# Optimization experiments

Hardware: AMD Instinct MI355X
Metric: run time of the kernel (lower is better)

Reference implementation:

```python
import jax, jax.numpy as jnp
import numpy as np

QBITS = 8  # all quant points configured to 8-bit symmetric by default


def fake_quant(v, bits=QBITS):
    """Symmetric per-tensor fake quantize/dequantize with STE-compatible form."""
    qmax = float(2 ** (bits - 1) - 1)
    scale = jnp.maximum(jnp.max(jnp.abs(v)) / qmax, 1e-8)
    q = jnp.clip(jnp.round(v / scale), -qmax - 1.0, qmax) * scale
    # straight-through estimator (identity gradient)
    return v + jax.lax.stop_gradient(q - v)


def reorder_pt_to_haste(w):
    # PyTorch gate order (r,z,n) -> Haste order (z,r,n) along leading 3H axis
    h3 = w.shape[0] // 3
    return jnp.concatenate([w[h3:2 * h3], w[:h3], w[2 * h3:]], axis=0)


def setup_inputs() -> dict:
    key = jax.random.key(0)
    ks = jax.random.split(key, 6)
    T, B, I, H = 1024, 64, 256, 256
    s = 1.0 / np.sqrt(H)
    return {
        "x": jax.random.normal(ks[0], (T, B, I), dtype=jnp.float32),
        "weight_ih": jax.random.normal(ks[1], (3 * H, I), dtype=jnp.float32) * s,
        "weight_hh": jax.random.normal(ks[2], (3 * H, H), dtype=jnp.float32) * s,
        "bias_ih": jax.random.normal(ks[3], (3 * H,), dtype=jnp.float32) * s,
        "bias_hh": jax.random.normal(ks[4], (3 * H,), dtype=jnp.float32) * s,
        "h0": jax.random.normal(ks[5], (B, H), dtype=jnp.float32),
    }


def _quant_gru(x, weight_ih, weight_hh, bias_ih, bias_hh, h0):
    T, B, I = x.shape
    H = weight_hh.shape[1]
    # Haste layout: W [I,3H], R [H,3H], gate order (z,r,n)
    W = reorder_pt_to_haste(weight_ih).T   # [I, 3H]
    R = reorder_pt_to_haste(weight_hh).T   # [H, 3H]
    bx = reorder_pt_to_haste(bias_ih)      # [3H]
    br = reorder_pt_to_haste(bias_hh)      # [3H]

    # per-tensor fake quant of inputs / weights / biases
    xq = fake_quant(x)
    Wq = fake_quant(W)
    Rq = fake_quant(R)
    bxq = fake_quant(bx)
    brq = fake_quant(br)

    # precompute Wx for all timesteps: [T,B,3H], quantized matmul output
    Wx = fake_quant(jnp.einsum('tbi,ih->tbh', xq, Wq))

    bx_z, bx_r, bx_n = bxq[:H], bxq[H:2 * H], bxq[2 * H:]
    br_z, br_r, br_n = brq[:H], brq[H:2 * H], brq[2 * H:]

    def step(h, wx_t):
        hq = fake_quant(h)
        Rh = fake_quant(hq @ Rq)           # [B, 3H]
        Rh_z, Rh_r, Rh_n = Rh[:, :H], Rh[:, H:2 * H], Rh[:, 2 * H:]
        wx_z, wx_r, wx_n = wx_t[:, :H], wx_t[:, H:2 * H], wx_t[:, 2 * H:]

        z_pre = fake_quant(wx_z + bx_z + Rh_z + br_z)
        z = fake_quant(jax.nn.sigmoid(z_pre))
        r_pre = fake_quant(wx_r + bx_r + Rh_r + br_r)
        r = fake_quant(jax.nn.sigmoid(r_pre))

        Rh_add_br = fake_quant(Rh_n + br_n)
        rRh = fake_quant(r * Rh_add_br)
        g_pre = fake_quant(wx_n + bx_n + rRh)
        g = fake_quant(jnp.tanh(g_pre))

        old_contrib = fake_quant(z * h)
        new_contrib = fake_quant((1.0 - z) * g)
        h_new = old_contrib + new_contrib
        return h_new, h_new

    h_last, output = jax.lax.scan(step, h0, Wx)  # output: [T, B, H]
    return output, h_last[None]  # h_n: [1, B, H]


def reference(x, weight_ih, weight_hh, bias_ih, bias_hh, h0):
    return _quant_gru(x, weight_ih, weight_hh, bias_ih, bias_hh, h0)
```

## Files before the change

kernel.cpp:

```cpp
#include <hip/hip_runtime.h>
#include <cstdint>
#include <cstddef>


typedef int   v4i __attribute__((ext_vector_type(4)));
typedef float v4f __attribute__((ext_vector_type(4)));

#define T_STEPS 1024
#define OUT_MAIN_FLOATS (1024*64*256)
#define WXQ_DOUT_OFF 16842752

__device__ __forceinline__ float clamp128(float x) {
  return fminf(fmaxf(x, -128.0f), 127.0f);
}
__device__ __forceinline__ int permj(int j) {
  return j < 256 ? j + 256 : (j < 512 ? j - 256 : j);
}
__device__ __forceinline__ float sigmoidf_(float x) {
  return __fdividef(1.0f, 1.0f + __expf(-x));
}
__device__ __forceinline__ float tanhf_(float x) {
  float e = __expf(-2.0f * fabsf(x));
  float t = __fdividef(1.0f - e, 1.0f + e);
  return copysignf(t, x);
}
__device__ __forceinline__ unsigned skey(float x) {
  unsigned u = __float_as_uint(x);
  return (u & 0x80000000u) ? ~u : (u | 0x80000000u);
}
__device__ __forceinline__ float sdec(unsigned k) {
  unsigned u = (k & 0x80000000u) ? (k ^ 0x80000000u) : ~k;
  return __uint_as_float(u);
}
__device__ __forceinline__ float wave_amax(float v) {
  #pragma unroll
  for (int m = 1; m <= 32; m <<= 1) v = fmaxf(v, __shfl_xor(v, m, 64));
  return v;
}

#define MFMA_I8(a, b, c) __builtin_amdgcn_mfma_i32_16x16x64_i8(a, b, c, 0, 0, 0)

__global__ void k_absmax(const float* __restrict__ p, int n4, unsigned* slot) {
  int i = blockIdx.x * blockDim.x + threadIdx.x;
  int stride = gridDim.x * blockDim.x;
  const v4f* p4 = (const v4f*)p;
  float m = 0.0f;
  for (; i < n4; i += stride) {
    v4f v = p4[i];
    m = fmaxf(m, fmaxf(fmaxf(fabsf(v[0]), fabsf(v[1])),
                       fmaxf(fabsf(v[2]), fabsf(v[3]))));
  }
  m = wave_amax(m);
  if ((threadIdx.x & 63) == 0) atomicMax(slot, __float_as_uint(m));
}

__global__ void k_frag(const float* __restrict__ src,
                       const unsigned* __restrict__ slots, int slot_idx,
                       signed char* __restrict__ dst) {
  int id = blockIdx.x * 256 + threadIdx.x;
  float s = fmaxf(__uint_as_float(slots[slot_idx]) / 127.0f, 1e-8f);
  int bq   = id & 3;
  int lane = (id >> 2) & 63;
  int kc   = (id >> 8) & 3;
  int ct   = id >> 10;
  int n = ct * 16 + (lane & 15);
  int k = kc * 64 + (lane >> 4) * 16 + bq * 4;
  const float* p = src + permj(n) * 256 + k;
  int b0 = ((int)clamp128(rintf(p[0] / s))) & 255;
  int b1 = ((int)clamp128(rintf(p[1] / s))) & 255;
  int b2 = ((int)clamp128(rintf(p[2] / s))) & 255;
  int b3 = ((int)clamp128(rintf(p[3] / s))) & 255;
  ((int*)dst)[id] = b0 | (b1 << 8) | (b2 << 16) | (b3 << 24);
}

__global__ void k_bias(const float* __restrict__ bih, const float* __restrict__ bhh,
                       const unsigned* __restrict__ slots, float* __restrict__ bqo) {
  int j = threadIdx.x;
  float s_bx = fmaxf(__uint_as_float(slots[3]) / 127.0f, 1e-8f);
  float s_br = fmaxf(__uint_as_float(slots[4]) / 127.0f, 1e-8f);
  int pr = permj(j);
  bqo[j]       = s_bx * clamp128(rintf(bih[pr] / s_bx));
  bqo[768 + j] = s_br * clamp128(rintf(bhh[pr] / s_br));
}

__global__ void k_xq(const float* __restrict__ x, const unsigned* __restrict__ slots,
                     signed char* __restrict__ xq8, int n4) {
  int i = blockIdx.x * blockDim.x + threadIdx.x;
  if (i >= n4) return;
  float s_x = fmaxf(__uint_as_float(slots[0]) / 127.0f, 1e-8f);
  v4f v = ((const v4f*)x)[i];
  int b0 = ((int)clamp128(rintf(v[0] / s_x))) & 255;
  int b1 = ((int)clamp128(rintf(v[1] / s_x))) & 255;
  int b2 = ((int)clamp128(rintf(v[2] / s_x))) & 255;
  int b3 = ((int)clamp128(rintf(v[3] / s_x))) & 255;
  ((int*)xq8)[i] = b0 | (b1 << 8) | (b2 << 16) | (b3 << 24);
}

__global__ __launch_bounds__(1024) void k_wx_i8(
    const signed char* __restrict__ xq8, const signed char* __restrict__ wf,
    unsigned* __restrict__ slots, signed char* __restrict__ wxq, int mode) {
  const int t = blockIdx.x;
  const int tid = threadIdx.x, lane = tid & 63, w = tid >> 6;
  const int cl = lane & 15, lh = lane >> 4;

  v4i Bz[4], Br[4], Bn[4];
  #pragma unroll
  for (int kc = 0; kc < 4; ++kc) {
    Bz[kc] = *(const v4i*)(wf + (((w)*4      + kc) * 64 + lane) * 16);
    Br[kc] = *(const v4i*)(wf + (((w + 16)*4 + kc) * 64 + lane) * 16);
    Bn[kc] = *(const v4i*)(wf + (((w + 32)*4 + kc) * 64 + lane) * 16);
  }
  v4i acc[3][4];
  #pragma unroll
  for (int p = 0; p < 3; ++p)
    #pragma unroll
    for (int rt = 0; rt < 4; ++rt) acc[p][rt] = (v4i){0, 0, 0, 0};

  const signed char* xr = xq8 + t * 16384;
  #pragma unroll
  for (int kc = 0; kc < 4; ++kc)
    #pragma unroll
    for (int rt = 0; rt < 4; ++rt) {
      v4i A = *(const v4i*)(xr + (rt * 16 + cl) * 256 + kc * 64 + lh * 16);
      acc[0][rt] = MFMA_I8(A, Bz[kc], acc[0][rt]);
      acc[1][rt] = MFMA_I8(A, Br[kc], acc[1][rt]);
      acc[2][rt] = MFMA_I8(A, Bn[kc], acc[2][rt]);
    }

  if (mode == 0) {
    int mm = 0;
    #pragma unroll
    for (int p = 0; p < 3; ++p)
      #pragma unroll
      for (int rt = 0; rt < 4; ++rt)
        #pragma unroll
        for (int rg = 0; rg < 4; ++rg) mm = max(mm, abs(acc[p][rt][rg]));
    #pragma unroll
    for (int m = 1; m <= 32; m <<= 1) mm = max(mm, __shfl_xor(mm, m, 64));
    if (lane == 0) atomicMax((int*)(slots + 5), mm);
  } else {
    int islot = *(const int*)(slots + 5);
    float maxMf = (float)islot;
    float s_x = fmaxf(__uint_as_float(slots[0]) / 127.0f, 1e-8f);
    float s_W = fmaxf(__uint_as_float(slots[1]) / 127.0f, 1e-8f);
    float s_xW = s_x * s_W;
    float s_wx = fmaxf(s_xW * maxMf / 127.0f, 1e-8f);
    #pragma unroll
    for (int p = 0; p < 3; ++p)
      #pragma unroll
      for (int rt = 0; rt < 4; ++rt) {
        int dw = 0;
        #pragma unroll
        for (int rg = 0; rg < 4; ++rg) {
          float qf = clamp128(rintf((s_xW * (float)acc[p][rt][rg]) / s_wx));
          dw |= (((int)qf) & 255) << (rg * 8);
        }
        ((int*)wxq)[t * 12288 + p * 4096 + rt * 1024 + w * 64 + lh * 16 + cl] = dw;
      }
  }
}

template <int NCH>
__device__ __forceinline__ void xchg(unsigned* keys, unsigned tag,
    unsigned (*lred)[8], unsigned long long* gslot, int wg, int tid, int lane) {
  const int rset = tag % 3;
  #pragma unroll
  for (int c = 0; c < NCH; ++c) {
    unsigned v = keys[c];
    #pragma unroll
    for (int m = 1; m <= 32; m <<= 1)
      v = max(v, (unsigned)__shfl_xor((int)v, m, 64));
    keys[c] = v;
  }
  if (lane == 0) {
    #pragma unroll
    for (int c = 0; c < NCH; ++c) atomicMax(&lred[rset][c], keys[c]);
  }
  __syncthreads();
  const int par = tag & 1;
  if (tid < NCH) {
    unsigned long long v =
        ((unsigned long long)tag << 32) | (unsigned long long)lred[rset][tid];
    __hip_atomic_store(&gslot[(par * 4 + wg) * 8 + tid], v,
                       __ATOMIC_RELAXED, __HIP_MEMORY_SCOPE_AGENT);
  } else if (tid == 32) {
    int ns = rset + 1; if (ns == 3) ns = 0;
    #pragma unroll
    for (int c = 0; c < 8; ++c) lred[ns][c] = 0u;
  } else if (tid >= 64 && tid < 64 + 3 * NCH) {
    int idx = tid - 64;
    int owi = idx / NCH;
    int c = idx - owi * NCH;
    int ow = owi + (owi >= wg ? 1 : 0);
    unsigned long long* p = &gslot[(par * 4 + ow) * 8 + c];
    unsigned long long v;
    do {
      v = __hip_atomic_load(p, __ATOMIC_RELAXED, __HIP_MEMORY_SCOPE_AGENT);
    } while ((unsigned)(v >> 32) != tag);
    atomicMax(&lred[rset][c], (unsigned)v);
  }
  __syncthreads();
  #pragma unroll
  for (int c = 0; c < NCH; ++c) keys[c] = lred[rset][c];
}

__global__ __launch_bounds__(1024) void k_recur4b(
    const signed char* __restrict__ wxq, const signed char* __restrict__ brf,
    const float* __restrict__ bq, const unsigned* __restrict__ slots,
    const float* __restrict__ h0p, float* __restrict__ out,
    unsigned long long* __restrict__ gslot) {
  __shared__ signed char ah[16 * 272];
  __shared__ unsigned lred[3][8];

  const int tid = threadIdx.x;
  const int lane = tid & 63;
  const int w = tid >> 6;
  const int cl = lane & 15;
  const int lh = lane >> 4;
  const int wg = blockIdx.x;
  const int j = w * 16 + cl;
  const int brow = wg * 16 + lh * 4;

  if (tid < 24) ((unsigned*)lred)[tid] = 0u;

  float s_x = fmaxf(__uint_as_float(slots[0]) / 127.0f, 1e-8f);
  float s_W = fmaxf(__uint_as_float(slots[1]) / 127.0f, 1e-8f);
  float s_R = fmaxf(__uint_as_float(slots[2]) / 127.0f, 1e-8f);
  float maxM0 = (float)(*(const int*)(slots + 5));
  float s_wx = fmaxf(s_x * s_W * maxM0 / 127.0f, 1e-8f);

  float bxz = bq[j], bxr = bq[j + 256], bxn = bq[j + 512];
  float brz = bq[768 + j], brr = bq[1024 + j], brn = bq[1280 + j];

  v4i Bz[4], Br[4], Bn[4];
  #pragma unroll
  for (int kc = 0; kc < 4; ++kc) {
    Bz[kc] = *(const v4i*)(brf + (((w)*4      + kc) * 64 + lane) * 16);
    Br[kc] = *(const v4i*)(brf + (((w + 16)*4 + kc) * 64 + lane) * 16);
    Bn[kc] = *(const v4i*)(brf + (((w + 32)*4 + kc) * 64 + lane) * 16);
  }

  float h[4];
  #pragma unroll
  for (int rg = 0; rg < 4; ++rg) h[rg] = h0p[(brow + rg) * 256 + j];

  __syncthreads();

  unsigned tag = 1;
  float sh;
  {
    float m = fmaxf(fmaxf(fabsf(h[0]), fabsf(h[1])),
                    fmaxf(fabsf(h[2]), fabsf(h[3])));
    unsigned kk[1] = {__float_as_uint(m)};
    xchg<1>(kk, tag++, lred, gslot, wg, tid, lane);
    sh = fmaxf(__uint_as_float(kk[0]) / 127.0f, 1e-8f);
    float ish = 1.0f / sh;
    #pragma unroll
    for (int rg = 0; rg < 4; ++rg)
      ah[(lh * 4 + rg) * 272 + j] = (signed char)(int)rintf(h[rg] * ish);
    __syncthreads();
  }

  for (int t = 0; t < T_STEPS; ++t) {
    const signed char* wb = wxq + (size_t)t * 49152 + (wg << 12) + (tid << 2);
    int wvz = *(const int*)(wb);
    int wvr = *(const int*)(wb + 16384);
    int wvn = *(const int*)(wb + 32768);

    v4i az4 = {0,0,0,0}, ar4 = {0,0,0,0}, an4 = {0,0,0,0};
    #pragma unroll
    for (int kc = 0; kc < 4; ++kc) {
      v4i A = *(const v4i*)(ah + cl * 272 + kc * 64 + lh * 16);
      az4 = MFMA_I8(A, Bz[kc], az4);
      ar4 = MFMA_I8(A, Br[kc], ar4);
      an4 = MFMA_I8(A, Bn[kc], an4);
    }

    int mm = 0;
    #pragma unroll
    for (int rg = 0; rg < 4; ++rg)
      mm = max(mm, max(abs(az4[rg]), max(abs(ar4[rg]), abs(an4[rg]))));
    unsigned kk[5];
    kk[0] = (unsigned)mm;
    xchg<1>(kk, tag++, lred, gslot, wg, tid, lane);
    float maxMf = (float)(int)kk[0];
    float s_Rh = fmaxf(sh * s_R * maxMf / 127.0f, 1e-8f);
    float fRh = (sh * s_R) / s_Rh;

    float zp[4], rp[4], nb[4];
    float az = 0.0f, ar = 0.0f, an = 0.0f;
    float mzs = -3.402823466e38f, mrs = -3.402823466e38f;
    #pragma unroll
    for (int rg = 0; rg < 4; ++rg) {
      float Rz = s_Rh * rintf((float)az4[rg] * fRh);
      float Rr = s_Rh * rintf((float)ar4[rg] * fRh);
      float Rn = s_Rh * rintf((float)an4[rg] * fRh);
      float wz = s_wx * (float)((signed char)(wvz >> (rg * 8)));
      float wr = s_wx * (float)((signed char)(wvr >> (rg * 8)));
      float a1 = ((wz + bxz) + Rz) + brz;
      float a2 = ((wr + bxr) + Rr) + brr;
      float a3 = Rn + brn;
      zp[rg] = a1; rp[rg] = a2; nb[rg] = a3;
      az = fmaxf(az, fabsf(a1)); ar = fmaxf(ar, fabsf(a2));
      an = fmaxf(an, fabsf(a3));
      mzs = fmaxf(mzs, a1); mrs = fmaxf(mrs, a2);
    }
    kk[0] = __float_as_uint(az); kk[1] = __float_as_uint(ar);
    kk[2] = __float_as_uint(an); kk[3] = skey(mzs); kk[4] = skey(mrs);
    xchg<5>(kk, tag++, lred, gslot, wg, tid, lane);
    float s1 = fmaxf(__uint_as_float(kk[0]) / 127.0f, 1e-8f), i1 = 1.0f / s1;
    float s2 = fmaxf(__uint_as_float(kk[1]) / 127.0f, 1e-8f), i2 = 1.0f / s2;
    float s3 = fmaxf(__uint_as_float(kk[2]) / 127.0f, 1e-8f), i3 = 1.0f / s3;
    float zq_max = s1 * rintf(sdec(kk[3]) * i1);
    float rq_max = s2 * rintf(sdec(kk[4]) * i2);
    float s4 = fmaxf(sigmoidf_(zq_max) / 127.0f, 1e-8f), i4 = 1.0f / s4;
    float s5 = fmaxf(sigmoidf_(rq_max) / 127.0f, 1e-8f), i5 = 1.0f / s5;

    float zf[4], rr_[4];
    float m6 = 0.0f;
    #pragma unroll
    for (int rg = 0; rg < 4; ++rg) {
      float zq = s1 * rintf(zp[rg] * i1);
      float rq = s2 * rintf(rp[rg] * i2);
      float zv = sigmoidf_(zq);
      float rv = sigmoidf_(rq);
      zf[rg] = s4 * rintf(zv * i4);
      float rq2 = s5 * rintf(rv * i5);
      float nbq = s3 * rintf(nb[rg] * i3);
      float rr = rq2 * nbq;
      rr_[rg] = rr;
      m6 = fmaxf(m6, fabsf(rr));
    }
    kk[0] = __float_as_uint(m6);
    xchg<1>(kk, tag++, lred, gslot, wg, tid, lane);
    float s6 = fmaxf(__uint_as_float(kk[0]) / 127.0f, 1e-8f), i6 = 1.0f / s6;

    float gp[4];
    float m7 = 0.0f;
    #pragma unroll
    for (int rg = 0; rg < 4; ++rg) {
      float rrq = s6 * rintf(rr_[rg] * i6);
      float wn = s_wx * (float)((signed char)(wvn >> (rg * 8)));
      float g = (wn + bxn) + rrq;
      gp[rg] = g;
      m7 = fmaxf(m7, fabsf(g));
    }
    kk[0] = __float_as_uint(m7);
    xchg<1>(kk, tag++, lred, gslot, wg, tid, lane);
    float m7g = __uint_as_float(kk[0]);
    float s7 = fmaxf(m7g / 127.0f, 1e-8f), i7 = 1.0f / s7;
    float gq_max = s7 * rintf(m7g * i7);
    float s8 = fmaxf(tanhf_(gq_max) / 127.0f, 1e-8f), i8v = 1.0f / s8;

    float ov[4], nv[4];
    float mo = 0.0f, mn = 0.0f;
    #pragma unroll
    for (int rg = 0; rg < 4; ++rg) {
      float gpq = s7 * rintf(gp[rg] * i7);
      float gv = tanhf_(gpq);
      float gq = s8 * rintf(gv * i8v);
      float o = zf[rg] * h[rg];
      float n = (1.0f - zf[rg]) * gq;
      ov[rg] = o; nv[rg] = n;
      mo = fmaxf(mo, fabsf(o)); mn = fmaxf(mn, fabsf(n));
    }
    kk[0] = __float_as_uint(mo); kk[1] = __float_as_uint(mn);
    xchg<2>(kk, tag++, lred, gslot, wg, tid, lane);
    float s9  = fmaxf(__uint_as_float(kk[0]) / 127.0f, 1e-8f), i9  = 1.0f / s9;
    float s10 = fmaxf(__uint_as_float(kk[1]) / 127.0f, 1e-8f), i10 = 1.0f / s10;

    float mh = 0.0f;
    #pragma unroll
    for (int rg = 0; rg < 4; ++rg) {
      float oq = s9  * rintf(ov[rg] * i9);
      float nq = s10 * rintf(nv[rg] * i10);
      float hn = oq + nq;
      h[rg] = hn;
      mh = fmaxf(mh, fabsf(hn));
      out[t * 16384 + (brow + rg) * 256 + j] = hn;
    }
    kk[0] = __float_as_uint(mh);
    xchg<1>(kk, tag++, lred, gslot, wg, tid, lane);
    sh = fmaxf(__uint_as_float(kk[0]) / 127.0f, 1e-8f);
    float ish = 1.0f / sh;
    #pragma unroll
    for (int rg = 0; rg < 4; ++rg)
      ah[(lh * 4 + rg) * 272 + j] = (signed char)(int)rintf(h[rg] * ish);
    __syncthreads();
  }

  #pragma unroll
  for (int rg = 0; rg < 4; ++rg)
    out[OUT_MAIN_FLOATS + (brow + rg) * 256 + j] = h[rg];
}

extern "C" void kernel_launch(void* const* d_in, const int* in_sizes, int n_in,
                              void* d_out, int out_size, void* d_ws, size_t ws_size,
                              hipStream_t stream) {
  const float* x   = (const float*)d_in[0];
  const float* wih = (const float*)d_in[1];
  const float* whh = (const float*)d_in[2];
  const float* bih = (const float*)d_in[3];
  const float* bhh = (const float*)d_in[4];
  const float* h0  = (const float*)d_in[5];
  float* out = (float*)d_out;

  unsigned* slots = (unsigned*)d_ws;
  unsigned long long* gslot = (unsigned long long*)((char*)d_ws + 512);
  float* bq       = (float*)((char*)d_ws + 4096);
  signed char* F  = (signed char*)d_ws + 10240;

  signed char* wxq = (signed char*)d_out + WXQ_DOUT_OFF;
  signed char* xq8 = (signed char*)d_out;

  hipMemsetAsync(d_ws, 0, 4096, stream);

  k_absmax<<<dim3(1024), dim3(256), 0, stream>>>(x,   16777216 / 4, slots + 0);
  k_absmax<<<dim3(96),   dim3(256), 0, stream>>>(wih, 196608 / 4,   slots + 1);
  k_absmax<<<dim3(96),   dim3(256), 0, stream>>>(whh, 196608 / 4,   slots + 2);
  k_absmax<<<dim3(1),    dim3(256), 0, stream>>>(bih, 768 / 4,      slots + 3);
  k_absmax<<<dim3(1),    dim3(256), 0, stream>>>(bhh, 768 / 4,      slots + 4);

  k_frag<<<dim3(192), dim3(256), 0, stream>>>(wih, slots, 1, F);
  k_bias<<<dim3(1), dim3(768), 0, stream>>>(bih, bhh, slots, bq);
  k_xq<<<dim3(16384), dim3(256), 0, stream>>>(x, slots, xq8, 4194304);

  k_wx_i8<<<dim3(1024), dim3(1024), 0, stream>>>(xq8, F, slots, wxq, 0);
  k_wx_i8<<<dim3(1024), dim3(1024), 0, stream>>>(xq8, F, slots, wxq, 1);

  k_frag<<<dim3(192), dim3(256), 0, stream>>>(whh, slots, 2, F);

  k_recur4b<<<dim3(4), dim3(1024), 0, stream>>>(wxq, F, bq, slots, h0, out,
                                                gslot);
}
```

Before: 14.14 ms.

## Split recurrent GRU kernel across 16 workgroups of 4 batch rows each

Re-partitions the sequential recurrence from 4 workgroups of 1024 threads (16 batch rows each) to 16 workgroups of 512 threads (4 batch rows each, padded to a 16-row MFMA tile with zeros). Each wave now computes two column tiles and stages MFMA results in shared memory so threads can handle 2 rows each. The grid-wide absmax exchange now waits on 15 peers instead of 3 per reduction. This spreads the per-step work over more compute units but wastes MFMA work on padding rows and raises cross-workgroup synchronization cost at each of the seven exchanges per step.

```diff
diff --git a/kernel.cpp b/kernel.cpp
--- a/kernel.cpp
+++ b/kernel.cpp
@@ -9,6 +9,7 @@
 #define T_STEPS 1024
 #define OUT_MAIN_FLOATS (1024*64*256)
 #define WXQ_DOUT_OFF 16842752
+#define NWG 16
 
 __device__ __forceinline__ float clamp128(float x) {
   return fminf(fmaxf(x, -128.0f), 127.0f);
@@ -181,18 +182,18 @@
   if (tid < NCH) {
     unsigned long long v =
         ((unsigned long long)tag << 32) | (unsigned long long)lred[rset][tid];
-    __hip_atomic_store(&gslot[(par * 4 + wg) * 8 + tid], v,
+    __hip_atomic_store(&gslot[(par * NWG + wg) * 8 + tid], v,
                        __ATOMIC_RELAXED, __HIP_MEMORY_SCOPE_AGENT);
   } else if (tid == 32) {
     int ns = rset + 1; if (ns == 3) ns = 0;
     #pragma unroll
     for (int c = 0; c < 8; ++c) lred[ns][c] = 0u;
-  } else if (tid >= 64 && tid < 64 + 3 * NCH) {
+  } else if (tid >= 64 && tid < 64 + (NWG - 1) * NCH) {
     int idx = tid - 64;
     int owi = idx / NCH;
     int c = idx - owi * NCH;
     int ow = owi + (owi >= wg ? 1 : 0);
-    unsigned long long* p = &gslot[(par * 4 + ow) * 8 + c];
+    unsigned long long* p = &gslot[(par * NWG + ow) * 8 + c];
     unsigned long long v;
     do {
       v = __hip_atomic_load(p, __ATOMIC_RELAXED, __HIP_MEMORY_SCOPE_AGENT);
@@ -204,12 +205,15 @@
   for (int c = 0; c < NCH; ++c) keys[c] = lred[rset][c];
 }
 
-__global__ __launch_bounds__(1024) void k_recur4b(
+__global__ __launch_bounds__(512, 1) void k_recur16(
     const signed char* __restrict__ wxq, const signed char* __restrict__ brf,
     const float* __restrict__ bq, const unsigned* __restrict__ slots,
     const float* __restrict__ h0p, float* __restrict__ out,
     unsigned long long* __restrict__ gslot) {
   __shared__ signed char ah[16 * 272];
+  __shared__ int zs[4 * 256];
+  __shared__ int rs_[4 * 256];
+  __shared__ int ns_[4 * 256];
   __shared__ unsigned lred[3][8];
 
   const int tid = threadIdx.x;
@@ -218,10 +222,11 @@
   const int cl = lane & 15;
   const int lh = lane >> 4;
   const int wg = blockIdx.x;
-  const int j = w * 16 + cl;
-  const int brow = wg * 16 + lh * 4;
+  const int j = tid & 255;
+  const int rp = (tid >> 8) * 2;
 
   if (tid < 24) ((unsigned*)lred)[tid] = 0u;
+  for (int i = tid; i < 1088; i += 512) ((int*)ah)[i] = 0;
 
   float s_x = fmaxf(__uint_as_float(slots[0]) / 127.0f, 1e-8f);
   float s_W = fmaxf(__uint_as_float(slots[1]) / 127.0f, 1e-8f);
@@ -232,54 +237,81 @@
   float bxz = bq[j], bxr = bq[j + 256], bxn = bq[j + 512];
   float brz = bq[768 + j], brr = bq[1024 + j], brn = bq[1280 + j];
 
-  v4i Bz[4], Br[4], Bn[4];
-  #pragma unroll
-  for (int kc = 0; kc < 4; ++kc) {
-    Bz[kc] = *(const v4i*)(brf + (((w)*4      + kc) * 64 + lane) * 16);
-    Br[kc] = *(const v4i*)(brf + (((w + 16)*4 + kc) * 64 + lane) * 16);
-    Bn[kc] = *(const v4i*)(brf + (((w + 32)*4 + kc) * 64 + lane) * 16);
-  }
-
-  float h[4];
-  #pragma unroll
-  for (int rg = 0; rg < 4; ++rg) h[rg] = h0p[(brow + rg) * 256 + j];
+  v4i Bz[2][4], Br[2][4], Bn[2][4];
+  #pragma unroll
+  for (int cg = 0; cg < 2; ++cg) {
+    int ct = w * 2 + cg;
+    #pragma unroll
+    for (int kc = 0; kc < 4; ++kc) {
+      Bz[cg][kc] = *(const v4i*)(brf + ((ct * 4        + kc) * 64 + lane) * 16);
+      Br[cg][kc] = *(const v4i*)(brf + (((ct + 16) * 4 + kc) * 64 + lane) * 16);
+      Bn[cg][kc] = *(const v4i*)(brf + (((ct + 32) * 4 + kc) * 64 + lane) * 16);
+    }
+  }
+
+  float h[2];
+  #pragma unroll
+  for (int s = 0; s < 2; ++s)
+    h[s] = h0p[(wg * 4 + rp + s) * 256 + j];
 
   __syncthreads();
 
   unsigned tag = 1;
   float sh;
   {
-    float m = fmaxf(fmaxf(fabsf(h[0]), fabsf(h[1])),
-                    fmaxf(fabsf(h[2]), fabsf(h[3])));
+    float m = fmaxf(fabsf(h[0]), fabsf(h[1]));
     unsigned kk[1] = {__float_as_uint(m)};
     xchg<1>(kk, tag++, lred, gslot, wg, tid, lane);
     sh = fmaxf(__uint_as_float(kk[0]) / 127.0f, 1e-8f);
     float ish = 1.0f / sh;
     #pragma unroll
-    for (int rg = 0; rg < 4; ++rg)
-      ah[(lh * 4 + rg) * 272 + j] = (signed char)(int)rintf(h[rg] * ish);
+    for (int s = 0; s < 2; ++s)
+      ah[(rp + s) * 272 + j] = (signed char)(int)rintf(h[s] * ish);
     __syncthreads();
   }
 
+  const int widx0 = (wg >> 2) * 1024 + (j >> 4) * 64 + (wg & 3) * 16 + (j & 15);
+
   for (int t = 0; t < T_STEPS; ++t) {
-    const signed char* wb = wxq + (size_t)t * 49152 + (wg << 12) + (tid << 2);
-    int wvz = *(const int*)(wb);
-    int wvr = *(const int*)(wb + 16384);
-    int wvn = *(const int*)(wb + 32768);
-
-    v4i az4 = {0,0,0,0}, ar4 = {0,0,0,0}, an4 = {0,0,0,0};
+    const int* wxi = (const int*)wxq + (size_t)t * 12288 + widx0;
+    int wvz = wxi[0];
+    int wvr = wxi[4096];
+    int wvn = wxi[8192];
+
+    v4i aZ[2] = {(v4i){0,0,0,0}, (v4i){0,0,0,0}};
+    v4i aR[2] = {(v4i){0,0,0,0}, (v4i){0,0,0,0}};
+    v4i aN[2] = {(v4i){0,0,0,0}, (v4i){0,0,0,0}};
     #pragma unroll
     for (int kc = 0; kc < 4; ++kc) {
       v4i A = *(const v4i*)(ah + cl * 272 + kc * 64 + lh * 16);
-      az4 = MFMA_I8(A, Bz[kc], az4);
-      ar4 = MFMA_I8(A, Br[kc], ar4);
-      an4 = MFMA_I8(A, Bn[kc], an4);
+      #pragma unroll
+      for (int cg = 0; cg < 2; ++cg) {
+        aZ[cg] = MFMA_I8(A, Bz[cg][kc], aZ[cg]);
+        aR[cg] = MFMA_I8(A, Br[cg][kc], aR[cg]);
+        aN[cg] = MFMA_I8(A, Bn[cg][kc], aN[cg]);
+      }
+    }
+
+    if (lane < 16) {
+      #pragma unroll
+      for (int cg = 0; cg < 2; ++cg) {
+        int jj = (w * 2 + cg) * 16 + lane;
+        #pragma unroll
+        for (int rg = 0; rg < 4; ++rg) {
+          zs[rg * 256 + jj] = aZ[cg][rg];
+          rs_[rg * 256 + jj] = aR[cg][rg];
+          ns_[rg * 256 + jj] = aN[cg][rg];
+        }
+      }
     }
 
     int mm = 0;
     #pragma unroll
-    for (int rg = 0; rg < 4; ++rg)
-      mm = max(mm, max(abs(az4[rg]), max(abs(ar4[rg]), abs(an4[rg]))));
+    for (int cg = 0; cg < 2; ++cg)
+      #pragma unroll
+      for (int rg = 0; rg < 4; ++rg)
+        mm = max(mm, max(abs(aZ[cg][rg]),
+                         max(abs(aR[cg][rg]), abs(aN[cg][rg]))));
     unsigned kk[5];
     kk[0] = (unsigned)mm;
     xchg<1>(kk, tag++, lred, gslot, wg, tid, lane);
@@ -287,20 +319,21 @@
     float s_Rh = fmaxf(sh * s_R * maxMf / 127.0f, 1e-8f);
     float fRh = (sh * s_R) / s_Rh;
 
-    float zp[4], rp[4], nb[4];
+    float zp[2], rpre[2], nb[2];
     float az = 0.0f, ar = 0.0f, an = 0.0f;
     float mzs = -3.402823466e38f, mrs = -3.402823466e38f;
     #pragma unroll
-    for (int rg = 0; rg < 4; ++rg) {
-      float Rz = s_Rh * rintf((float)az4[rg] * fRh);
-      float Rr = s_Rh * rintf((float)ar4[rg] * fRh);
-      float Rn = s_Rh * rintf((float)an4[rg] * fRh);
-      float wz = s_wx * (float)((signed char)(wvz >> (rg * 8)));
-      float wr = s_wx * (float)((signed char)(wvr >> (rg * 8)));
+    for (int s = 0; s < 2; ++s) {
+      int r = rp + s;
+      float Rz = s_Rh * rintf((float)zs[r * 256 + j] * fRh);
+      float Rr = s_Rh * rintf((float)rs_[r * 256 + j] * fRh);
+      float Rn = s_Rh * rintf((float)ns_[r * 256 + j] * fRh);
+      float wz = s_wx * (float)((signed char)(wvz >> (r * 8)));
+      float wr = s_wx * (float)((signed char)(wvr >> (r * 8)));
       float a1 = ((wz + bxz) + Rz) + brz;
       float a2 = ((wr + bxr) + Rr) + brr;
       float a3 = Rn + brn;
-      zp[rg] = a1; rp[rg] = a2; nb[rg] = a3;
+      zp[s] = a1; rpre[s] = a2; nb[s] = a3;
       az = fmaxf(az, fabsf(a1)); ar = fmaxf(ar, fabsf(a2));
       an = fmaxf(an, fabsf(a3));
       mzs = fmaxf(mzs, a1); mrs = fmaxf(mrs, a2);
@@ -316,33 +349,33 @@
     float s4 = fmaxf(sigmoidf_(zq_max) / 127.0f, 1e-8f), i4 = 1.0f / s4;
     float s5 = fmaxf(sigmoidf_(rq_max) / 127.0f, 1e-8f), i5 = 1.0f / s5;
 
-    float zf[4], rr_[4];
+    float zf[2], rr_[2];
     float m6 = 0.0f;
     #pragma unroll
-    for (int rg = 0; rg < 4; ++rg) {
-      float zq = s1 * rintf(zp[rg] * i1);
-      float rq = s2 * rintf(rp[rg] * i2);
+    for (int s = 0; s < 2; ++s) {
+      float zq = s1 * rintf(zp[s] * i1);
+      float rq = s2 * rintf(rpre[s] * i2);
       float zv = sigmoidf_(zq);
       float rv = sigmoidf_(rq);
-      zf[rg] = s4 * rintf(zv * i4);
+      zf[s] = s4 * rintf(zv * i4);
       float rq2 = s5 * rintf(rv * i5);
-      float nbq = s3 * rintf(nb[rg] * i3);
+      float nbq = s3 * rintf(nb[s] * i3);
       float rr = rq2 * nbq;
-      rr_[rg] = rr;
+      rr_[s] = rr;
       m6 = fmaxf(m6, fabsf(rr));
     }
     kk[0] = __float_as_uint(m6);
     xchg<1>(kk, tag++, lred, gslot, wg, tid, lane);
     float s6 = fmaxf(__uint_as_float(kk[0]) / 127.0f, 1e-8f), i6 = 1.0f / s6;
 
-    float gp[4];
+    float gp[2];
     float m7 = 0.0f;
     #pragma unroll
-    for (int rg = 0; rg < 4; ++rg) {
-      float rrq = s6 * rintf(rr_[rg] * i6);
-      float wn = s_wx * (float)((signed char)(wvn >> (rg * 8)));
+    for (int s = 0; s < 2; ++s) {
+      float rrq = s6 * rintf(rr_[s] * i6);
+      float wn = s_wx * (float)((signed char)(wvn >> ((rp + s) * 8)));
       float g = (wn + bxn) + rrq;
-      gp[rg] = g;
+      gp[s] = g;
       m7 = fmaxf(m7, fabsf(g));
     }
     kk[0] = __float_as_uint(m7);
@@ -352,16 +385,16 @@
     float gq_max = s7 * rintf(m7g * i7);
     float s8 = fmaxf(tanhf_(gq_max) / 127.0f, 1e-8f), i8v = 1.0f / s8;
 
-    float ov[4], nv[4];
+    float ov[2], nv[2];
     float mo = 0.0f, mn = 0.0f;
     #pragma unroll
-    for (int rg = 0; rg < 4; ++rg) {
-      float gpq = s7 * rintf(gp[rg] * i7);
+    for (int s = 0; s < 2; ++s) {
+      float gpq = s7 * rintf(gp[s] * i7);
       float gv = tanhf_(gpq);
       float gq = s8 * rintf(gv * i8v);
-      float o = zf[rg] * h[rg];
-      float n = (1.0f - zf[rg]) * gq;
-      ov[rg] = o; nv[rg] = n;
+      float o = zf[s] * h[s];
+      float n = (1.0f - zf[s]) * gq;
+      ov[s] = o; nv[s] = n;
       mo = fmaxf(mo, fabsf(o)); mn = fmaxf(mn, fabsf(n));
     }
     kk[0] = __float_as_uint(mo); kk[1] = __float_as_uint(mn);
@@ -371,27 +404,27 @@
 
     float mh = 0.0f;
     #pragma unroll
-    for (int rg = 0; rg < 4; ++rg) {
-      float oq = s9  * rintf(ov[rg] * i9);
-      float nq = s10 * rintf(nv[rg] * i10);
+    for (int s = 0; s < 2; ++s) {
+      float oq = s9  * rintf(ov[s] * i9);
+      float nq = s10 * rintf(nv[s] * i10);
       float hn = oq + nq;
-      h[rg] = hn;
+      h[s] = hn;
       mh = fmaxf(mh, fabsf(hn));
-      out[t * 16384 + (brow + rg) * 256 + j] = hn;
+      out[t * 16384 + (wg * 4 + rp + s) * 256 + j] = hn;
     }
     kk[0] = __float_as_uint(mh);
     xchg<1>(kk, tag++, lred, gslot, wg, tid, lane);
     sh = fmaxf(__uint_as_float(kk[0]) / 127.0f, 1e-8f);
     float ish = 1.0f / sh;
     #pragma unroll
-    for (int rg = 0; rg < 4; ++rg)
-      ah[(lh * 4 + rg) * 272 + j] = (signed char)(int)rintf(h[rg] * ish);
+    for (int s = 0; s < 2; ++s)
+      ah[(rp + s) * 272 + j] = (signed char)(int)rintf(h[s] * ish);
     __syncthreads();
   }
 
   #pragma unroll
-  for (int rg = 0; rg < 4; ++rg)
-    out[OUT_MAIN_FLOATS + (brow + rg) * 256 + j] = h[rg];
+  for (int s = 0; s < 2; ++s)
+    out[OUT_MAIN_FLOATS + (wg * 4 + rp + s) * 256 + j] = h[s];
 }
 
 extern "C" void kernel_launch(void* const* d_in, const int* in_sizes, int n_in,
@@ -430,6 +463,6 @@
 
   k_frag<<<dim3(192), dim3(256), 0, stream>>>(whh, slots, 2, F);
 
-  k_recur4b<<<dim3(4), dim3(1024), 0, stream>>>(wxq, F, bq, slots, h0, out,
-                                                gslot);
-}
+  k_recur16<<<dim3(NWG), dim3(512), 0, stream>>>(wxq, F, bq, slots, h0, out,
+                                                 gslot);
+}
```

Measured after the change: 14.27 ms. No clear change (+0.9%).

## Split recurrence across eight workgroups of 512 threads with LDS accumulator staging

Applied to the files above, without the earlier changes.

The persistent GRU recurrence now runs on 8 workgroups of 512 threads, each owning 8 batch rows, instead of 4 workgroups of 1024 threads owning 16 rows. Each wave computes two column tiles of MFMA with the top half of the 16-row A tile zero-padded, then stages the int32 accumulators in LDS so threads can read them in a row-major layout. Barriers are replaced by an explicit lgkmcnt-wait plus s_barrier, and the cross-workgroup amax exchange now spans 8 groups. The aim is shorter per-step critical paths per workgroup, paid for with wasted MFMA work, extra LDS traffic and more global-atomic exchange participants per step.

```diff
diff --git a/kernel.cpp b/kernel.cpp
--- a/kernel.cpp
+++ b/kernel.cpp
@@ -9,6 +9,7 @@
 #define T_STEPS 1024
 #define OUT_MAIN_FLOATS (1024*64*256)
 #define WXQ_DOUT_OFF 16842752
+#define NWG 8
 
 __device__ __forceinline__ float clamp128(float x) {
   return fminf(fmaxf(x, -128.0f), 127.0f);
@@ -36,6 +37,11 @@
   #pragma unroll
   for (int m = 1; m <= 32; m <<= 1) v = fmaxf(v, __shfl_xor(v, m, 64));
   return v;
+}
+
+__device__ __forceinline__ void bar_lgkm() {
+  asm volatile("s_waitcnt lgkmcnt(0)\n\ts_barrier" ::: "memory");
+  __builtin_amdgcn_sched_barrier(0);
 }
 
 #define MFMA_I8(a, b, c) __builtin_amdgcn_mfma_i32_16x16x64_i8(a, b, c, 0, 0, 0)
@@ -176,40 +182,43 @@
     #pragma unroll
     for (int c = 0; c < NCH; ++c) atomicMax(&lred[rset][c], keys[c]);
   }
-  __syncthreads();
+  bar_lgkm();
   const int par = tag & 1;
   if (tid < NCH) {
     unsigned long long v =
         ((unsigned long long)tag << 32) | (unsigned long long)lred[rset][tid];
-    __hip_atomic_store(&gslot[(par * 4 + wg) * 8 + tid], v,
+    __hip_atomic_store(&gslot[(par * NWG + wg) * 8 + tid], v,
                        __ATOMIC_RELAXED, __HIP_MEMORY_SCOPE_AGENT);
   } else if (tid == 32) {
     int ns = rset + 1; if (ns == 3) ns = 0;
     #pragma unroll
     for (int c = 0; c < 8; ++c) lred[ns][c] = 0u;
-  } else if (tid >= 64 && tid < 64 + 3 * NCH) {
+  } else if (tid >= 64 && tid < 64 + (NWG - 1) * NCH) {
     int idx = tid - 64;
     int owi = idx / NCH;
     int c = idx - owi * NCH;
     int ow = owi + (owi >= wg ? 1 : 0);
-    unsigned long long* p = &gslot[(par * 4 + ow) * 8 + c];
+    unsigned long long* p = &gslot[(par * NWG + ow) * 8 + c];
     unsigned long long v;
     do {
       v = __hip_atomic_load(p, __ATOMIC_RELAXED, __HIP_MEMORY_SCOPE_AGENT);
     } while ((unsigned)(v >> 32) != tag);
     atomicMax(&lred[rset][c], (unsigned)v);
   }
-  __syncthreads();
+  bar_lgkm();
   #pragma unroll
   for (int c = 0; c < NCH; ++c) keys[c] = lred[rset][c];
 }
 
-__global__ __launch_bounds__(1024) void k_recur4b(
+__global__ __launch_bounds__(512, 1) void k_recur8(
     const signed char* __restrict__ wxq, const signed char* __restrict__ brf,
     const float* __restrict__ bq, const unsigned* __restrict__ slots,
     const float* __restrict__ h0p, float* __restrict__ out,
     unsigned long long* __restrict__ gslot) {
   __shared__ signed char ah[16 * 272];
+  __shared__ int zs[8 * 256];
+  __shared__ int rs_[8 * 256];
+  __shared__ int ns_[8 * 256];
   __shared__ unsigned lred[3][8];
 
   const int tid = threadIdx.x;
@@ -218,10 +227,11 @@
   const int cl = lane & 15;
   const int lh = lane >> 4;
   const int wg = blockIdx.x;
-  const int j = w * 16 + cl;
-  const int brow = wg * 16 + lh * 4;
+  const int j = tid & 255;
+  const int rblk = tid >> 8;
 
   if (tid < 24) ((unsigned*)lred)[tid] = 0u;
+  for (int i = tid; i < 1088; i += 512) ((int*)ah)[i] = 0;
 
   float s_x = fmaxf(__uint_as_float(slots[0]) / 127.0f, 1e-8f);
   float s_W = fmaxf(__uint_as_float(slots[1]) / 127.0f, 1e-8f);
@@ -232,17 +242,22 @@
   float bxz = bq[j], bxr = bq[j + 256], bxn = bq[j + 512];
   float brz = bq[768 + j], brr = bq[1024 + j], brn = bq[1280 + j];
 
-  v4i Bz[4], Br[4], Bn[4];
-  #pragma unroll
-  for (int kc = 0; kc < 4; ++kc) {
-    Bz[kc] = *(const v4i*)(brf + (((w)*4      + kc) * 64 + lane) * 16);
-    Br[kc] = *(const v4i*)(brf + (((w + 16)*4 + kc) * 64 + lane) * 16);
-    Bn[kc] = *(const v4i*)(brf + (((w + 32)*4 + kc) * 64 + lane) * 16);
+  v4i Bz[2][4], Br[2][4], Bn[2][4];
+  #pragma unroll
+  for (int cg = 0; cg < 2; ++cg) {
+    int ct = w * 2 + cg;
+    #pragma unroll
+    for (int kc = 0; kc < 4; ++kc) {
+      Bz[cg][kc] = *(const v4i*)(brf + ((ct * 4        + kc) * 64 + lane) * 16);
+      Br[cg][kc] = *(const v4i*)(brf + (((ct + 16) * 4 + kc) * 64 + lane) * 16);
+      Bn[cg][kc] = *(const v4i*)(brf + (((ct + 32) * 4 + kc) * 64 + lane) * 16);
+    }
   }
 
   float h[4];
   #pragma unroll
-  for (int rg = 0; rg < 4; ++rg) h[rg] = h0p[(brow + rg) * 256 + j];
+  for (int rg = 0; rg < 4; ++rg)
+    h[rg] = h0p[(wg * 8 + rblk * 4 + rg) * 256 + j];
 
   __syncthreads();
 
@@ -257,29 +272,55 @@
     float ish = 1.0f / sh;
     #pragma unroll
     for (int rg = 0; rg < 4; ++rg)
-      ah[(lh * 4 + rg) * 272 + j] = (signed char)(int)rintf(h[rg] * ish);
-    __syncthreads();
-  }
+      ah[(rblk * 4 + rg) * 272 + j] = (signed char)(int)rintf(h[rg] * ish);
+    bar_lgkm();
+  }
+
+  const int rt_ = wg >> 1;
+  const int lhb = ((wg & 1) << 1) | rblk;
+  const int widx0 = rt_ * 1024 + (j >> 4) * 64 + lhb * 16 + (j & 15);
 
   for (int t = 0; t < T_STEPS; ++t) {
-    const signed char* wb = wxq + (size_t)t * 49152 + (wg << 12) + (tid << 2);
-    int wvz = *(const int*)(wb);
-    int wvr = *(const int*)(wb + 16384);
-    int wvn = *(const int*)(wb + 32768);
-
-    v4i az4 = {0,0,0,0}, ar4 = {0,0,0,0}, an4 = {0,0,0,0};
+    const int* wxi = (const int*)wxq + (size_t)t * 12288 + widx0;
+    int wvz = wxi[0];
+    int wvr = wxi[4096];
+    int wvn = wxi[8192];
+
+    v4i aZ[2] = {(v4i){0,0,0,0}, (v4i){0,0,0,0}};
+    v4i aR[2] = {(v4i){0,0,0,0}, (v4i){0,0,0,0}};
+    v4i aN[2] = {(v4i){0,0,0,0}, (v4i){0,0,0,0}};
     #pragma unroll
     for (int kc = 0; kc < 4; ++kc) {
       v4i A = *(const v4i*)(ah + cl * 272 + kc * 64 + lh * 16);
-      az4 = MFMA_I8(A, Bz[kc], az4);
-      ar4 = MFMA_I8(A, Br[kc], ar4);
-      an4 = MFMA_I8(A, Bn[kc], an4);
+      #pragma unroll
+      for (int cg = 0; cg < 2; ++cg) {
+        aZ[cg] = MFMA_I8(A, Bz[cg][kc], aZ[cg]);
+        aR[cg] = MFMA_I8(A, Br[cg][kc], aR[cg]);
+        aN[cg] = MFMA_I8(A, Bn[cg][kc], aN[cg]);
+      }
+    }
+
+    if (lane < 32) {
+      #pragma unroll
+      for (int cg = 0; cg < 2; ++cg) {
+        int jj = (w * 2 + cg) * 16 + cl;
+        #pragma unroll
+        for (int rg = 0; rg < 4; ++rg) {
+          int row = lh * 4 + rg;
+          zs[row * 256 + jj] = aZ[cg][rg];
+          rs_[row * 256 + jj] = aR[cg][rg];
+          ns_[row * 256 + jj] = aN[cg][rg];
+        }
+      }
     }
 
     int mm = 0;
     #pragma unroll
-    for (int rg = 0; rg < 4; ++rg)
-      mm = max(mm, max(abs(az4[rg]), max(abs(ar4[rg]), abs(an4[rg]))));
+    for (int cg = 0; cg < 2; ++cg)
+      #pragma unroll
+      for (int rg = 0; rg < 4; ++rg)
+        mm = max(mm, max(abs(aZ[cg][rg]),
+                         max(abs(aR[cg][rg]), abs(aN[cg][rg]))));
     unsigned kk[5];
     kk[0] = (unsigned)mm;
     xchg<1>(kk, tag++, lred, gslot, wg, tid, lane);
@@ -292,9 +333,10 @@
     float mzs = -3.402823466e38f, mrs = -3.402823466e38f;
     #pragma unroll
     for (int rg = 0; rg < 4; ++rg) {
-      float Rz = s_Rh * rintf((float)az4[rg] * fRh);
-      float Rr = s_Rh * rintf((float)ar4[rg] * fRh);
-      float Rn = s_Rh * rintf((float)an4[rg] * fRh);
+      int row = rblk * 4 + rg;
+      float Rz = s_Rh * rintf((float)zs[row * 256 + j] * fRh);
+      float Rr = s_Rh * rintf((float)rs_[row * 256 + j] * fRh);
+      float Rn = s_Rh * rintf((float)ns_[row * 256 + j] * fRh);
       float wz = s_wx * (float)((signed char)(wvz >> (rg * 8)));
       float wr = s_wx * (float)((signed char)(wvr >> (rg * 8)));
       float a1 = ((wz + bxz) + Rz) + brz;
@@ -377,7 +419,7 @@
       float hn = oq + nq;
       h[rg] = hn;
       mh = fmaxf(mh, fabsf(hn));
-      out[t * 16384 + (brow + rg) * 256 + j] = hn;
+      out[t * 16384 + (wg * 8 + rblk * 4 + rg) * 256 + j] = hn;
     }
     kk[0] = __float_as_uint(mh);
     xchg<1>(kk, tag++, lred, gslot, wg, tid, lane);
@@ -385,13 +427,13 @@
     float ish = 1.0f / sh;
     #pragma unroll
     for (int rg = 0; rg < 4; ++rg)
-      ah[(lh * 4 + rg) * 272 + j] = (signed char)(int)rintf(h[rg] * ish);
-    __syncthreads();
+      ah[(rblk * 4 + rg) * 272 + j] = (signed char)(int)rintf(h[rg] * ish);
+    bar_lgkm();
   }
 
   #pragma unroll
   for (int rg = 0; rg < 4; ++rg)
-    out[OUT_MAIN_FLOATS + (brow + rg) * 256 + j] = h[rg];
+    out[OUT_MAIN_FLOATS + (wg * 8 + rblk * 4 + rg) * 256 + j] = h[rg];
 }
 
 extern "C" void kernel_launch(void* const* d_in, const int* in_sizes, int n_in,
@@ -430,6 +472,6 @@
 
   k_frag<<<dim3(192), dim3(256), 0, stream>>>(whh, slots, 2, F);
 
-  k_recur4b<<<dim3(4), dim3(1024), 0, stream>>>(wxq, F, bq, slots, h0, out,
+  k_recur8<<<dim3(NWG), dim3(512), 0, stream>>>(wxq, F, bq, slots, h0, out,
                                                 gslot);
 }
```

After: 14.30 ms. No clear change (+1.1%).
